# Kernel tuning notes

Measured on AMD Instinct MI355X. Metric: run time of the kernel, lower is better.

## Reference

```python
import jax, jax.numpy as jnp
import numpy as np

B, T, D, H = 8, 1024, 512, 8
D4 = 4 * D
SIGMA = 16.0
EPS = 1e-5


def layer_norm(x, w, b):
    m = jnp.mean(x, axis=-1, keepdims=True)
    v = jnp.mean((x - m) ** 2, axis=-1, keepdims=True)
    return (x - m) * jax.lax.rsqrt(v + EPS) * w + b


def setup_inputs() -> dict:
    key = jax.random.key(0)
    ks = jax.random.split(key, 12)
    return {
        "x": jax.random.normal(ks[0], (B, T, D), jnp.float32),
        "posv": jax.random.randint(ks[1], (B, T), 0, 64, jnp.int32),
        "posh": jax.random.randint(ks[2], (B, T), 0, 64, jnp.int32),
        "norm1_w": jnp.ones((D,), jnp.float32),
        "norm1_b": jnp.zeros((D,), jnp.float32),
        "in_w": jax.random.normal(ks[3], (3 * D, D), jnp.float32) * (D ** -0.5),
        "in_b": jnp.zeros((3 * D,), jnp.float32),
        "out_w": jax.random.normal(ks[4], (D, D), jnp.float32) * (D ** -0.5),
        "out_b": jnp.zeros((D,), jnp.float32),
        "norm2_w": jnp.ones((D,), jnp.float32),
        "norm2_b": jnp.zeros((D,), jnp.float32),
        "w1": jax.random.normal(ks[5], (D4, D), jnp.float32) * (D ** -0.5),
        "b1": jnp.zeros((D4,), jnp.float32),
        "w2": jax.random.normal(ks[6], (D, D4), jnp.float32) * (D4 ** -0.5),
        "b2": jnp.zeros((D,), jnp.float32),
        "gate": jnp.array(0.0, jnp.float32),
    }


def reference(x, posv, posh, norm1_w, norm1_b, in_w, in_b, out_w, out_b,
              norm2_w, norm2_b, w1, b1, w2, b2, gate):
    hd = D // H
    residual = x
    xn = layer_norm(x, norm1_w, norm1_b)

    # --- standard multi-head self-attention (dropout=eval identity) ---
    qkv = xn @ in_w.T + in_b                       # [B,T,3D]
    q, k, v = jnp.split(qkv, 3, axis=-1)
    q = q.reshape(B, T, H, hd).transpose(0, 2, 1, 3)  # [B,H,T,hd]
    k = k.reshape(B, T, H, hd).transpose(0, 2, 1, 3)
    v = v.reshape(B, T, H, hd).transpose(0, 2, 1, 3)
    scores = jnp.einsum("bhqd,bhkd->bhqk", q, k) * (hd ** -0.5)
    attn = jax.nn.softmax(scores, axis=-1)
    ctx = jnp.einsum("bhqk,bhkd->bhqd", attn, v)   # [B,H,T,hd]
    ctx = ctx.transpose(0, 2, 1, 3).reshape(B, T, D)
    std_out = ctx @ out_w.T + out_b

    # --- Gaussian kernel position attention ---
    pos = jnp.stack([posv, posh], axis=-1).astype(jnp.float32)  # [B,T,2]
    dist_sq = jnp.sum((pos[:, :, None, :] - pos[:, None, :, :]) ** 2, axis=-1)  # [B,T,T]
    kw = jnp.exp(-dist_sq / (2.0 * SIGMA ** 2))
    kw = kw / jnp.sum(kw, axis=-1, keepdims=True)
    kernel_out = kw @ xn                            # [B,T,D]

    g = jax.nn.sigmoid(gate)
    x1 = residual + g * std_out + (1.0 - g) * kernel_out

    # --- MLP block ---
    xn2 = layer_norm(x1, norm2_w, norm2_b)
    h = jax.nn.gelu(xn2 @ w1.T + b1, approximate=False)
    return x1 + h @ w2.T + b2
```

## Files before the change

kernel.cpp:

```cpp
#include <hip/hip_runtime.h>
#include <hip/hip_bf16.h>
#include <math.h>

typedef unsigned short ushort_t;
typedef short short8 __attribute__((ext_vector_type(8)));
typedef float f32x4 __attribute__((ext_vector_type(4)));

__device__ __forceinline__ float b2f(ushort_t u) {
  union { unsigned u; float f; } v; v.u = ((unsigned)u) << 16; return v.f;
}
__device__ __forceinline__ ushort_t f2b(float f) {
  union { float f; unsigned u; } v; v.f = f;
  unsigned r = (v.u + 0x7FFFu + ((v.u >> 16) & 1u)) >> 16;
  return (ushort_t)r;
}
__device__ __forceinline__ ushort_t f2b_rtz(float f) {
  union { float f; unsigned u; } v; v.f = f;
  return (ushort_t)(v.u >> 16);
}
__device__ __forceinline__ float gelu_fast(float v) {
  float u = 0.7978845608f * (v + 0.044715f * v * v * v);
  float a = fabsf(u);
  float t = exp2f(a * -2.8853900817779268f);
  float th = (1.f - t) / (1.f + t);
  th = copysignf(th, u);
  return 0.5f * v * (1.f + th);
}

union U16x8 { uint4 v; ushort_t s[8]; };

typedef const __attribute__((address_space(1))) unsigned int glb_u32;
typedef __attribute__((address_space(3))) unsigned int lds_u32;
__device__ __forceinline__ void gl_lds16(const ushort_t* g, ushort_t* l) {
  __builtin_amdgcn_global_load_lds((glb_u32*)g, (lds_u32*)l, 16, 0, 0);
}

__global__ __launch_bounds__(256) void cvt4_kernel(const float* __restrict__ s0,
                                                   const float* __restrict__ s1,
                                                   const float* __restrict__ s2,
                                                   const float* __restrict__ s3,
                                                   ushort_t* __restrict__ d0,
                                                   ushort_t* __restrict__ d1,
                                                   ushort_t* __restrict__ d2,
                                                   ushort_t* __restrict__ d3) {
  long i = (long)blockIdx.x * 256 + threadIdx.x;
  const float* s; ushort_t* d; long off;
  if (i < 196608)       { s = s0; d = d0; off = i; }
  else if (i < 262144)  { s = s1; d = d1; off = i - 196608; }
  else if (i < 524288)  { s = s2; d = d2; off = i - 262144; }
  else                  { s = s3; d = d3; off = i - 524288; }
  float4 f = *(const float4*)(s + off * 4);
  union { uint2 v; ushort_t s[4]; } o;
  o.s[0] = f2b(f.x); o.s[1] = f2b(f.y); o.s[2] = f2b(f.z); o.s[3] = f2b(f.w);
  *(uint2*)(d + off * 4) = o.v;
}

__global__ __launch_bounds__(256) void ln_kernel(const float* __restrict__ x,
                                                 const float* __restrict__ w,
                                                 const float* __restrict__ b,
                                                 ushort_t* __restrict__ out) {
  int tid = threadIdx.x, wave = tid >> 6, lane = tid & 63;
  long token = (long)blockIdx.x * 4 + wave;
  const float* xr = x + token * 512 + lane * 8;
  float4 a0 = *(const float4*)xr;
  float4 a1 = *(const float4*)(xr + 4);
  float xf[8] = {a0.x, a0.y, a0.z, a0.w, a1.x, a1.y, a1.z, a1.w};
  float s = 0.f, sq = 0.f;
#pragma unroll
  for (int i = 0; i < 8; i++) { s += xf[i]; sq += xf[i] * xf[i]; }
#pragma unroll
  for (int off = 1; off < 64; off <<= 1) { s += __shfl_xor(s, off); sq += __shfl_xor(sq, off); }
  float m = s * (1.f / 512.f);
  float var = sq * (1.f / 512.f) - m * m;
  float rs = rsqrtf(var + 1e-5f);
  float4 w0 = *(const float4*)(w + lane * 8);
  float4 w1v = *(const float4*)(w + lane * 8 + 4);
  float4 b0 = *(const float4*)(b + lane * 8);
  float4 b1v = *(const float4*)(b + lane * 8 + 4);
  float wf[8] = {w0.x, w0.y, w0.z, w0.w, w1v.x, w1v.y, w1v.z, w1v.w};
  float bf[8] = {b0.x, b0.y, b0.z, b0.w, b1v.x, b1v.y, b1v.z, b1v.w};
  U16x8 o;
#pragma unroll
  for (int i = 0; i < 8; i++) o.s[i] = f2b((xf[i] - m) * rs * wf[i] + bf[i]);
  *(uint4*)(out + token * 512 + lane * 8) = o.v;
}

__global__ __launch_bounds__(256) void ln_b_kernel(const ushort_t* __restrict__ x,
                                                   const float* __restrict__ w,
                                                   const float* __restrict__ b,
                                                   ushort_t* __restrict__ out) {
  int tid = threadIdx.x, wave = tid >> 6, lane = tid & 63;
  long token = (long)blockIdx.x * 4 + wave;
  U16x8 ux; ux.v = *(const uint4*)(x + token * 512 + lane * 8);
  float xf[8], s = 0.f, sq = 0.f;
#pragma unroll
  for (int i = 0; i < 8; i++) { xf[i] = b2f(ux.s[i]); s += xf[i]; sq += xf[i] * xf[i]; }
#pragma unroll
  for (int off = 1; off < 64; off <<= 1) { s += __shfl_xor(s, off); sq += __shfl_xor(sq, off); }
  float m = s * (1.f / 512.f);
  float var = sq * (1.f / 512.f) - m * m;
  float rs = rsqrtf(var + 1e-5f);
  float4 w0 = *(const float4*)(w + lane * 8);
  float4 w1v = *(const float4*)(w + lane * 8 + 4);
  float4 b0 = *(const float4*)(b + lane * 8);
  float4 b1v = *(const float4*)(b + lane * 8 + 4);
  float wf[8] = {w0.x, w0.y, w0.z, w0.w, w1v.x, w1v.y, w1v.z, w1v.w};
  float bf[8] = {b0.x, b0.y, b0.z, b0.w, b1v.x, b1v.y, b1v.z, b1v.w};
  U16x8 o;
#pragma unroll
  for (int i = 0; i < 8; i++) o.s[i] = f2b((xf[i] - m) * rs * wf[i] + bf[i]);
  *(uint4*)(out + token * 512 + lane * 8) = o.v;
}

__global__ __launch_bounds__(256) void kw_kernel(const int* __restrict__ posv,
                                                 const int* __restrict__ posh,
                                                 ushort_t* __restrict__ kw) {
  int b = blockIdx.x >> 10, i = blockIdx.x & 1023;
  int tid = threadIdx.x;
  const int* pv = posv + b * 1024;
  const int* ph = posh + b * 1024;
  int pvi = pv[i], phi = ph[i];
  int j0 = tid * 4;
  int4 vj = *(const int4*)(pv + j0);
  int4 hj = *(const int4*)(ph + j0);
  int vv[4] = {vj.x, vj.y, vj.z, vj.w};
  int hh[4] = {hj.x, hj.y, hj.z, hj.w};
  float e[4]; float loc = 0.f;
#pragma unroll
  for (int u = 0; u < 4; u++) {
    int dv = pvi - vv[u], dh = phi - hh[u];
    e[u] = expf((float)(dv * dv + dh * dh) * (-1.f / 512.f));
    loc += e[u];
  }
#pragma unroll
  for (int off = 1; off < 64; off <<= 1) loc += __shfl_xor(loc, off);
  __shared__ float wsum[4];
  __shared__ float tot;
  if ((tid & 63) == 0) wsum[tid >> 6] = loc;
  __syncthreads();
  if (tid == 0) tot = wsum[0] + wsum[1] + wsum[2] + wsum[3];
  __syncthreads();
  float inv = 1.f / tot;
  union { uint2 v; ushort_t s[4]; } o;
#pragma unroll
  for (int u = 0; u < 4; u++) o.s[u] = f2b(e[u] * inv);
  *(uint2*)&kw[((long)(b * 1024 + i)) * 1024 + j0] = o.v;
}

__global__ __launch_bounds__(256) void tr_kernel(const ushort_t* __restrict__ in,
                                                 ushort_t* __restrict__ out,
                                                 int R, int C) {
  __shared__ ushort_t tile[64 * 64];
  int z = blockIdx.z, r0 = blockIdx.y * 64, c0 = blockIdx.x * 64;
  const ushort_t* src = in + (long)z * R * C;
  ushort_t* dst = out + (long)z * R * C;
  int tid = threadIdx.x;
  int tr = tid >> 2;
  const ushort_t* s = src + (long)(r0 + tr) * C + c0;
  int g = (tr + (tr >> 4)) & 7;
#pragma unroll
  for (int u = 0; u < 2; u++) {
    int c = (tid & 3) + u * 4;
    *(uint4*)&tile[tr * 64 + (c ^ g) * 8] = *(const uint4*)(s + c * 8);
  }
  __syncthreads();
  int oc = tid >> 2, ob = (tid & 3) * 16;
  U16x8 o0, o1;
#pragma unroll
  for (int j = 0; j < 16; j++) {
    int r = ob + j;
    int gg = (r + (r >> 4)) & 7;
    ushort_t val = tile[r * 64 + (((oc >> 3) ^ gg)) * 8 + (oc & 7)];
    if (j < 8) o0.s[j] = val; else o1.s[j - 8] = val;
  }
  ushort_t* d = dst + (long)(c0 + oc) * R + r0 + ob;
  *(uint4*)d = o0.v;
  *(uint4*)(d + 8) = o1.v;
}

struct GemmP {
  const ushort_t* A; const ushort_t* Bm;
  long sA, sB, sC;
  int lda, ldb, ldc, K;
  const float* biasf;
  const float* residf;
  const ushort_t* auxb;
  const float* auxf;
  float* outf;
  ushort_t* outb;
  ushort_t* qp; ushort_t* kp; ushort_t* vp;
  const float* gate;
};

template <int BM, int BN, int EPI>
__global__ __launch_bounds__(256) void gemm_k(GemmP p) {
  constexpr int TI = BM / 32, TJ = BN / 32;
  constexpr int RA = BM / 64, RB = BN / 64;
  __shared__ ushort_t As[2][BM * 32];
  __shared__ ushort_t Bs[2][BN * 32];
  int tid = threadIdx.x, wv = tid >> 6, lane = tid & 63;
  int quad = lane >> 4, l15 = lane & 15;
  int bl = blockIdx.x + gridDim.x * blockIdx.y;
  int m0 = (bl % gridDim.y) * BM;
  int n0 = (bl / gridDim.y) * BN;
  int z = blockIdx.z;
  const ushort_t* A = p.A + (long)z * p.sA;
  const ushort_t* Bm = p.Bm + (long)z * p.sB;
  int wm = (wv & 1) * (BM / 2), wn = (wv >> 1) * (BN / 2);
  f32x4 acc[TI][TJ];
#pragma unroll
  for (int i = 0; i < TI; i++)
#pragma unroll
    for (int j = 0; j < TJ; j++)
#pragma unroll
      for (int r = 0; r < 4; r++) acc[i][j][r] = 0.f;

  int srow = tid >> 2;
  int sc = ((tid & 3) ^ ((tid >> 3) & 3)) * 8;
  const ushort_t* ga = A + (long)(m0 + srow) * p.lda + sc;
  const ushort_t* gb = Bm + (long)(n0 + srow) * p.ldb + sc;
  long a64 = (long)64 * p.lda, b64 = (long)64 * p.ldb;
  int aswz = (quad ^ ((l15 >> 1) & 3)) * 8;
  int nsteps = p.K >> 5;

#pragma unroll
  for (int rr = 0; rr < RA; rr++)
    gl_lds16(ga + rr * a64, As[0] + rr * 2048 + wv * 512);
#pragma unroll
  for (int rr = 0; rr < RB; rr++)
    gl_lds16(gb + rr * b64, Bs[0] + rr * 2048 + wv * 512);
  __syncthreads();

  for (int ks = 0; ks < nsteps; ks++) {
    int cur = ks & 1;
    if (ks + 1 < nsteps) {
      const ushort_t* a0 = ga + (ks + 1) * 32;
      const ushort_t* b0 = gb + (ks + 1) * 32;
#pragma unroll
      for (int rr = 0; rr < RA; rr++)
        gl_lds16(a0 + rr * a64, As[cur ^ 1] + rr * 2048 + wv * 512);
#pragma unroll
      for (int rr = 0; rr < RB; rr++)
        gl_lds16(b0 + rr * b64, Bs[cur ^ 1] + rr * 2048 + wv * 512);
    }
    short8 av[TI], bv[TJ];
#pragma unroll
    for (int ti = 0; ti < TI; ti++)
      av[ti] = *(const short8*)&As[cur][(wm + ti * 16 + l15) * 32 + aswz];
#pragma unroll
    for (int tj = 0; tj < TJ; tj++)
      bv[tj] = *(const short8*)&Bs[cur][(wn + tj * 16 + l15) * 32 + aswz];
#pragma unroll
    for (int ti = 0; ti < TI; ti++)
#pragma unroll
      for (int tj = 0; tj < TJ; tj++)
        acc[ti][tj] = __builtin_amdgcn_mfma_f32_16x16x32_bf16(av[ti], bv[tj], acc[ti][tj], 0, 0, 0);
    __syncthreads();
  }

  float g = 0.f;
  if constexpr (EPI == 2) g = 1.f / (1.f + expf(-p.gate[0]));
#pragma unroll
  for (int ti = 0; ti < TI; ti++) {
#pragma unroll
    for (int tj = 0; tj < TJ; tj++) {
#pragma unroll
      for (int r = 0; r < 4; r++) {
        int gm = m0 + wm + ti * 16 + quad * 4 + r;
        int n = n0 + wn + tj * 16 + l15;
        float v = acc[ti][tj][r];
        if constexpr (EPI == 0) {
          v += p.biasf[n];
          int bb = gm >> 10, tt = gm & 1023;
          if (n < 512) {
            int h = n >> 6, d = n & 63;
            p.qp[((long)(bb * 8 + h) * 1024 + tt) * 64 + d] = f2b(v);
          } else if (n < 1024) {
            int n2 = n - 512, h = n2 >> 6, d = n2 & 63;
            p.kp[((long)(bb * 8 + h) * 1024 + tt) * 64 + d] = f2b(v);
          } else {
            int n2 = n - 1024, h = n2 >> 6, d = n2 & 63;
            p.vp[((long)(bb * 8 + h) * 1024 + tt) * 64 + d] = f2b(v);
          }
        } else if constexpr (EPI == 1) {
          p.outb[(long)z * p.sC + (long)gm * p.ldc + n] = f2b(v);
        } else if constexpr (EPI == 2) {
          v += p.biasf[n];
          long idx = (long)gm * 512 + n;
          p.outb[idx] = f2b(p.residf[idx] + g * v + (1.f - g) * b2f(p.auxb[idx]));
        } else if constexpr (EPI == 3) {
          v += p.biasf[n];
          p.outb[(long)gm * p.ldc + n] = f2b(gelu_fast(v));
        } else {
          v += p.biasf[n];
          long idx = (long)gm * 512 + n;
          p.outf[idx] = v + b2f(p.auxb[idx]);
        }
      }
    }
  }
}

__global__ __launch_bounds__(256) void flash_k(const ushort_t* __restrict__ q,
                                               const ushort_t* __restrict__ k,
                                               const ushort_t* __restrict__ vT,
                                               ushort_t* __restrict__ ctx) {
  int bl = blockIdx.x + gridDim.x * blockIdx.y;
  int bh = bl % 64;
  int q0 = (bl / 64) * 128;
  int tid = threadIdx.x, wv = tid >> 6, lane = tid & 63;
  int quad = lane >> 4, l15 = lane & 15;
  __shared__ ushort_t Qs[128 * 64], Ks[2][64 * 64], Vt[2][64 * 64], Ps[128 * 64];
  int wm = wv * 32;

  int srow = tid >> 3;
  int sc = ((tid & 7) ^ ((tid >> 3) & 7)) * 8;
#pragma unroll
  for (int e = 0; e < 4; e++) {
    const ushort_t* gq = &q[((long)bh * 1024 + q0 + e * 32 + srow) * 64 + sc];
    gl_lds16(gq, Qs + e * 2048 + wv * 512);
  }
#pragma unroll
  for (int e = 0; e < 2; e++) {
    const ushort_t* gk = &k[((long)bh * 1024 + e * 32 + srow) * 64 + sc];
    gl_lds16(gk, Ks[0] + e * 2048 + wv * 512);
    const ushort_t* gv = &vT[((long)bh * 64 + e * 32 + srow) * 1024 + sc];
    gl_lds16(gv, Vt[0] + e * 2048 + wv * 512);
  }
  __syncthreads();

  f32x4 O[2][4];
#pragma unroll
  for (int ti = 0; ti < 2; ti++)
#pragma unroll
    for (int t = 0; t < 4; t++)
#pragma unroll
      for (int r = 0; r < 4; r++) O[ti][t][r] = 0.f;
  float lsum[2][4] = {{0.f, 0.f, 0.f, 0.f}, {0.f, 0.f, 0.f, 0.f}};

  const float SC = 0.18033688011112042f;
  for (int kt = 0; kt < 16; kt++) {
    int cur = kt & 1;
    if (kt + 1 < 16) {
#pragma unroll
      for (int e = 0; e < 2; e++) {
        const ushort_t* gk = &k[((long)bh * 1024 + (kt + 1) * 64 + e * 32 + srow) * 64 + sc];
        gl_lds16(gk, Ks[cur ^ 1] + e * 2048 + wv * 512);
        const ushort_t* gv = &vT[((long)bh * 64 + e * 32 + srow) * 1024 + (kt + 1) * 64 + sc];
        gl_lds16(gv, Vt[cur ^ 1] + e * 2048 + wv * 512);
      }
    }
#pragma unroll
    for (int ti = 0; ti < 2; ti++) {
      f32x4 S[4];
#pragma unroll
      for (int t = 0; t < 4; t++) {
#pragma unroll
        for (int r = 0; r < 4; r++) S[t][r] = 0.f;
#pragma unroll
        for (int kk = 0; kk < 2; kk++) {
          short8 a = *(const short8*)&Qs[(wm + ti * 16 + l15) * 64 + ((kk * 4 + quad) ^ (l15 & 7)) * 8];
          short8 bfrag = *(const short8*)&Ks[cur][(t * 16 + l15) * 64 + ((kk * 4 + quad) ^ (l15 & 7)) * 8];
          S[t] = __builtin_amdgcn_mfma_f32_16x16x32_bf16(a, bfrag, S[t], 0, 0, 0);
        }
      }
#pragma unroll
      for (int t = 0; t < 4; t++) {
#pragma unroll
        for (int r = 0; r < 4; r++) {
          float pv = exp2f(S[t][r] * SC);
          lsum[ti][r] += pv;
          int row = wm + ti * 16 + quad * 4 + r;
          Ps[row * 64 + ((2 * t + (l15 >> 3)) ^ (row & 7)) * 8 + (l15 & 7)] = f2b_rtz(pv);
        }
      }
    }
#pragma unroll
    for (int ti = 0; ti < 2; ti++) {
#pragma unroll
      for (int t = 0; t < 4; t++) {
#pragma unroll
        for (int kk = 0; kk < 2; kk++) {
          short8 a = *(const short8*)&Ps[(wm + ti * 16 + l15) * 64 + ((kk * 4 + quad) ^ (l15 & 7)) * 8];
          short8 bfrag = *(const short8*)&Vt[cur][(t * 16 + l15) * 64 + ((kk * 4 + quad) ^ (l15 & 7)) * 8];
          O[ti][t] = __builtin_amdgcn_mfma_f32_16x16x32_bf16(a, bfrag, O[ti][t], 0, 0, 0);
        }
      }
    }
    __syncthreads();
  }
#pragma unroll
  for (int ti = 0; ti < 2; ti++)
#pragma unroll
    for (int r = 0; r < 4; r++) {
#pragma unroll
      for (int off = 1; off < 16; off <<= 1) lsum[ti][r] += __shfl_xor(lsum[ti][r], off);
    }
  int bb = bh >> 3, h = bh & 7;
#pragma unroll
  for (int ti = 0; ti < 2; ti++) {
#pragma unroll
    for (int r = 0; r < 4; r++) {
      float inv = 1.f / lsum[ti][r];
      long row = (long)bb * 1024 + q0 + wm + ti * 16 + quad * 4 + r;
#pragma unroll
      for (int t = 0; t < 4; t++)
        ctx[row * 512 + h * 64 + t * 16 + l15] = f2b(O[ti][t][r] * inv);
    }
  }
}

extern "C" void kernel_launch(void* const* d_in, const int* in_sizes, int n_in,
                              void* d_out, int out_size, void* d_ws, size_t ws_size,
                              hipStream_t stream) {
  const float* x    = (const float*)d_in[0];
  const int* posv   = (const int*)d_in[1];
  const int* posh   = (const int*)d_in[2];
  const float* n1w  = (const float*)d_in[3];
  const float* n1b  = (const float*)d_in[4];
  const float* in_w = (const float*)d_in[5];
  const float* in_b = (const float*)d_in[6];
  const float* outw = (const float*)d_in[7];
  const float* outb = (const float*)d_in[8];
  const float* n2w  = (const float*)d_in[9];
  const float* n2b  = (const float*)d_in[10];
  const float* w1   = (const float*)d_in[11];
  const float* b1   = (const float*)d_in[12];
  const float* w2   = (const float*)d_in[13];
  const float* b2   = (const float*)d_in[14];
  const float* gate = (const float*)d_in[15];
  float* out = (float*)d_out;

  char* ws = (char*)d_ws;
  const size_t MB = 1024 * 1024;
  ushort_t* q    = (ushort_t*)(ws + 0 * MB);
  ushort_t* kk   = (ushort_t*)(ws + 8 * MB);
  ushort_t* vtmp = (ushort_t*)(ws + 16 * MB);
  ushort_t* vT   = (ushort_t*)(ws + 24 * MB);
  ushort_t* kw   = (ushort_t*)(ws + 32 * MB);
  ushort_t* xn   = (ushort_t*)(ws + 48 * MB);
  ushort_t* xnT  = (ushort_t*)(ws + 56 * MB);
  ushort_t* ctx  = (ushort_t*)(ws + 64 * MB);
  ushort_t* ko   = (ushort_t*)(ws + 72 * MB);
  ushort_t* x1b  = (ushort_t*)(ws + 80 * MB);
  ushort_t* xn2  = (ushort_t*)(ws + 16 * MB);
  ushort_t* inwb = (ushort_t*)(ws + 96 * MB);
  ushort_t* owb  = (ushort_t*)(ws + 98 * MB);
  ushort_t* w1b  = (ushort_t*)(ws + 99 * MB);
  ushort_t* w2b  = (ushort_t*)(ws + 101 * MB);
  ushort_t* h    = (ushort_t*)(ws + 24 * MB);

  cvt4_kernel<<<3072, 256, 0, stream>>>(in_w, outw, w1, w2, inwb, owb, w1b, w2b);
  ln_kernel<<<2048, 256, 0, stream>>>(x, n1w, n1b, xn);
  kw_kernel<<<8192, 256, 0, stream>>>(posv, posh, kw);
  {
    GemmP p = {};
    p.A = xn; p.Bm = inwb; p.lda = 512; p.ldb = 512; p.K = 512;
    p.biasf = in_b; p.qp = q; p.kp = kk; p.vp = vtmp;
    gemm_k<128, 128, 0><<<dim3(12, 64, 1), 256, 0, stream>>>(p);
  }
  tr_kernel<<<dim3(1, 16, 64), 256, 0, stream>>>(vtmp, vT, 1024, 64);
  flash_k<<<dim3(8, 64, 1), 256, 0, stream>>>(q, kk, vT, ctx);
  tr_kernel<<<dim3(8, 16, 8), 256, 0, stream>>>(xn, xnT, 1024, 512);
  {
    GemmP p = {};
    p.A = kw; p.Bm = xnT; p.lda = 1024; p.ldb = 1024; p.ldc = 512; p.K = 1024;
    p.sA = 1024L * 1024; p.sB = 512L * 1024; p.sC = 1024L * 512;
    p.outb = ko;
    gemm_k<64, 128, 1><<<dim3(4, 16, 8), 256, 0, stream>>>(p);
  }
  {
    GemmP p = {};
    p.A = ctx; p.Bm = owb; p.lda = 512; p.ldb = 512; p.K = 512;
    p.biasf = outb; p.residf = x; p.auxb = ko; p.outb = x1b; p.gate = gate;
    gemm_k<64, 64, 2><<<dim3(8, 128, 1), 256, 0, stream>>>(p);
  }
  ln_b_kernel<<<2048, 256, 0, stream>>>(x1b, n2w, n2b, xn2);
  {
    GemmP p = {};
    p.A = xn2; p.Bm = w1b; p.lda = 512; p.ldb = 512; p.ldc = 2048; p.K = 512;
    p.biasf = b1; p.outb = h;
    gemm_k<128, 128, 3><<<dim3(16, 64, 1), 256, 0, stream>>>(p);
  }
  {
    GemmP p = {};
    p.A = h; p.Bm = w2b; p.lda = 2048; p.ldb = 2048; p.K = 2048;
    p.biasf = b2; p.auxb = x1b; p.outf = out;
    gemm_k<64, 128, 4><<<dim3(4, 128, 1), 256, 0, stream>>>(p);
  }
}
```

Baseline: 308.4 us.

## Compute transposed S in flash attention, keep Q in registers, prescale Q

The flash attention kernel now computes S^T, with K as the A operand and Q fragments held in registers instead of LDS. Each lane therefore owns a query row, so P can be packed into bf16 pairs with perm and stored to LDS with 8-byte writes, and the row sum needs only two shuffles. The softmax scale is folded into Q in the QKV GEMM epilogue, which removes a multiply per score. The costs are extra registers and a change in rounding, since Q is now rounded to bf16 after scaling.

After: 298.8 us. -3.1%, faster.

```diff
diff --git a/kernel.cpp b/kernel.cpp
--- a/kernel.cpp
+++ b/kernel.cpp
@@ -13,10 +13,6 @@
   union { float f; unsigned u; } v; v.f = f;
   unsigned r = (v.u + 0x7FFFu + ((v.u >> 16) & 1u)) >> 16;
   return (ushort_t)r;
-}
-__device__ __forceinline__ ushort_t f2b_rtz(float f) {
-  union { float f; unsigned u; } v; v.f = f;
-  return (ushort_t)(v.u >> 16);
 }
 __device__ __forceinline__ float gelu_fast(float v) {
   float u = 0.7978845608f * (v + 0.044715f * v * v * v);
@@ -274,7 +270,7 @@
           int bb = gm >> 10, tt = gm & 1023;
           if (n < 512) {
             int h = n >> 6, d = n & 63;
-            p.qp[((long)(bb * 8 + h) * 1024 + tt) * 64 + d] = f2b(v);
+            p.qp[((long)(bb * 8 + h) * 1024 + tt) * 64 + d] = f2b(v * 0.18033688011112042f);
           } else if (n < 1024) {
             int n2 = n - 512, h = n2 >> 6, d = n2 & 63;
             p.kp[((long)(bb * 8 + h) * 1024 + tt) * 64 + d] = f2b(v);
@@ -310,102 +306,102 @@
   int q0 = (bl / 64) * 128;
   int tid = threadIdx.x, wv = tid >> 6, lane = tid & 63;
   int quad = lane >> 4, l15 = lane & 15;
-  __shared__ ushort_t Qs[128 * 64], Ks[2][64 * 64], Vt[2][64 * 64], Ps[128 * 64];
+  __shared__ ushort_t Ks[2][64 * 64], Vt[2][64 * 64];
+  __shared__ ushort_t Pt[128 * 64];
   int wm = wv * 32;
+
+  short8 qf[2][2];
+#pragma unroll
+  for (int tq = 0; tq < 2; tq++)
+#pragma unroll
+    for (int kk = 0; kk < 2; kk++)
+      qf[tq][kk] = *(const short8*)&q[((long)bh * 1024 + q0 + wm + tq * 16 + l15) * 64 + kk * 32 + quad * 8];
 
   int srow = tid >> 3;
   int sc = ((tid & 7) ^ ((tid >> 3) & 7)) * 8;
 #pragma unroll
-  for (int e = 0; e < 4; e++) {
-    const ushort_t* gq = &q[((long)bh * 1024 + q0 + e * 32 + srow) * 64 + sc];
-    gl_lds16(gq, Qs + e * 2048 + wv * 512);
-  }
-#pragma unroll
   for (int e = 0; e < 2; e++) {
-    const ushort_t* gk = &k[((long)bh * 1024 + e * 32 + srow) * 64 + sc];
-    gl_lds16(gk, Ks[0] + e * 2048 + wv * 512);
-    const ushort_t* gv = &vT[((long)bh * 64 + e * 32 + srow) * 1024 + sc];
-    gl_lds16(gv, Vt[0] + e * 2048 + wv * 512);
+    gl_lds16(&k[((long)bh * 1024 + e * 32 + srow) * 64 + sc], Ks[0] + e * 2048 + wv * 512);
+    gl_lds16(&vT[((long)bh * 64 + e * 32 + srow) * 1024 + sc], Vt[0] + e * 2048 + wv * 512);
   }
   __syncthreads();
 
   f32x4 O[2][4];
 #pragma unroll
-  for (int ti = 0; ti < 2; ti++)
-#pragma unroll
-    for (int t = 0; t < 4; t++)
-#pragma unroll
-      for (int r = 0; r < 4; r++) O[ti][t][r] = 0.f;
-  float lsum[2][4] = {{0.f, 0.f, 0.f, 0.f}, {0.f, 0.f, 0.f, 0.f}};
-
-  const float SC = 0.18033688011112042f;
+  for (int tq = 0; tq < 2; tq++)
+#pragma unroll
+    for (int td = 0; td < 4; td++)
+#pragma unroll
+      for (int r = 0; r < 4; r++) O[tq][td][r] = 0.f;
+  float ls[2] = {0.f, 0.f};
+
+  int pswz = (l15 & 7) << 1;
   for (int kt = 0; kt < 16; kt++) {
     int cur = kt & 1;
     if (kt + 1 < 16) {
 #pragma unroll
       for (int e = 0; e < 2; e++) {
-        const ushort_t* gk = &k[((long)bh * 1024 + (kt + 1) * 64 + e * 32 + srow) * 64 + sc];
-        gl_lds16(gk, Ks[cur ^ 1] + e * 2048 + wv * 512);
-        const ushort_t* gv = &vT[((long)bh * 64 + e * 32 + srow) * 1024 + (kt + 1) * 64 + sc];
-        gl_lds16(gv, Vt[cur ^ 1] + e * 2048 + wv * 512);
+        gl_lds16(&k[((long)bh * 1024 + (kt + 1) * 64 + e * 32 + srow) * 64 + sc], Ks[cur ^ 1] + e * 2048 + wv * 512);
+        gl_lds16(&vT[((long)bh * 64 + e * 32 + srow) * 1024 + (kt + 1) * 64 + sc], Vt[cur ^ 1] + e * 2048 + wv * 512);
       }
     }
 #pragma unroll
-    for (int ti = 0; ti < 2; ti++) {
+    for (int tq = 0; tq < 2; tq++) {
       f32x4 S[4];
 #pragma unroll
-      for (int t = 0; t < 4; t++) {
-#pragma unroll
-        for (int r = 0; r < 4; r++) S[t][r] = 0.f;
+      for (int tk = 0; tk < 4; tk++) {
+#pragma unroll
+        for (int r = 0; r < 4; r++) S[tk][r] = 0.f;
 #pragma unroll
         for (int kk = 0; kk < 2; kk++) {
-          short8 a = *(const short8*)&Qs[(wm + ti * 16 + l15) * 64 + ((kk * 4 + quad) ^ (l15 & 7)) * 8];
-          short8 bfrag = *(const short8*)&Ks[cur][(t * 16 + l15) * 64 + ((kk * 4 + quad) ^ (l15 & 7)) * 8];
-          S[t] = __builtin_amdgcn_mfma_f32_16x16x32_bf16(a, bfrag, S[t], 0, 0, 0);
+          short8 kf = *(const short8*)&Ks[cur][(tk * 16 + l15) * 64 + ((kk * 4 + quad) ^ (l15 & 7)) * 8];
+          S[tk] = __builtin_amdgcn_mfma_f32_16x16x32_bf16(kf, qf[tq][kk], S[tk], 0, 0, 0);
         }
       }
 #pragma unroll
-      for (int t = 0; t < 4; t++) {
-#pragma unroll
-        for (int r = 0; r < 4; r++) {
-          float pv = exp2f(S[t][r] * SC);
-          lsum[ti][r] += pv;
-          int row = wm + ti * 16 + quad * 4 + r;
-          Ps[row * 64 + ((2 * t + (l15 >> 3)) ^ (row & 7)) * 8 + (l15 & 7)] = f2b_rtz(pv);
+      for (int tk = 0; tk < 4; tk++) {
+        float p0 = exp2f(S[tk][0]);
+        float p1 = exp2f(S[tk][1]);
+        float p2 = exp2f(S[tk][2]);
+        float p3 = exp2f(S[tk][3]);
+        ls[tq] += (p0 + p1) + (p2 + p3);
+        unsigned lo = __builtin_amdgcn_perm(__float_as_uint(p1), __float_as_uint(p0), 0x07060302u);
+        unsigned hi = __builtin_amdgcn_perm(__float_as_uint(p3), __float_as_uint(p2), 0x07060302u);
+        int gnum = (tk * 4 + quad) ^ pswz;
+        uint2 pr; pr.x = lo; pr.y = hi;
+        *(uint2*)&Pt[(wm + tq * 16 + l15) * 64 + gnum * 4] = pr;
+      }
+    }
+#pragma unroll
+    for (int tq = 0; tq < 2; tq++) {
+#pragma unroll
+      for (int kk = 0; kk < 2; kk++) {
+        short8 pf = *(const short8*)&Pt[(wm + tq * 16 + l15) * 64 + (((kk * 8 + quad * 2) ^ pswz)) * 4];
+#pragma unroll
+        for (int td = 0; td < 4; td++) {
+          short8 vf = *(const short8*)&Vt[cur][(td * 16 + l15) * 64 + ((kk * 4 + quad) ^ (l15 & 7)) * 8];
+          O[tq][td] = __builtin_amdgcn_mfma_f32_16x16x32_bf16(pf, vf, O[tq][td], 0, 0, 0);
         }
       }
     }
-#pragma unroll
-    for (int ti = 0; ti < 2; ti++) {
-#pragma unroll
-      for (int t = 0; t < 4; t++) {
-#pragma unroll
-        for (int kk = 0; kk < 2; kk++) {
-          short8 a = *(const short8*)&Ps[(wm + ti * 16 + l15) * 64 + ((kk * 4 + quad) ^ (l15 & 7)) * 8];
-          short8 bfrag = *(const short8*)&Vt[cur][(t * 16 + l15) * 64 + ((kk * 4 + quad) ^ (l15 & 7)) * 8];
-          O[ti][t] = __builtin_amdgcn_mfma_f32_16x16x32_bf16(a, bfrag, O[ti][t], 0, 0, 0);
-        }
-      }
-    }
     __syncthreads();
   }
 #pragma unroll
-  for (int ti = 0; ti < 2; ti++)
+  for (int tq = 0; tq < 2; tq++) {
+    ls[tq] += __shfl_xor(ls[tq], 16);
+    ls[tq] += __shfl_xor(ls[tq], 32);
+  }
+  int bb = bh >> 3, h = bh & 7;
+#pragma unroll
+  for (int tq = 0; tq < 2; tq++) {
 #pragma unroll
     for (int r = 0; r < 4; r++) {
-#pragma unroll
-      for (int off = 1; off < 16; off <<= 1) lsum[ti][r] += __shfl_xor(lsum[ti][r], off);
-    }
-  int bb = bh >> 3, h = bh & 7;
-#pragma unroll
-  for (int ti = 0; ti < 2; ti++) {
-#pragma unroll
-    for (int r = 0; r < 4; r++) {
-      float inv = 1.f / lsum[ti][r];
-      long row = (long)bb * 1024 + q0 + wm + ti * 16 + quad * 4 + r;
-#pragma unroll
-      for (int t = 0; t < 4; t++)
-        ctx[row * 512 + h * 64 + t * 16 + l15] = f2b(O[ti][t][r] * inv);
+      int qrow = quad * 4 + r;
+      float inv = 1.f / __shfl(ls[tq], (lane & 48) | qrow);
+      long row = (long)bb * 1024 + q0 + wm + tq * 16 + qrow;
+#pragma unroll
+      for (int td = 0; td < 4; td++)
+        ctx[row * 512 + h * 64 + td * 16 + l15] = f2b(O[tq][td][r] * inv);
     }
   }
 }
```
